# Kernel tuning notes

Hardware: AMD Instinct MI355X
Metric: run time of the kernel (lower is better)

Reference implementation:

```python
import jax, jax.numpy as jnp
import numpy as np

NEG_INF = float('-inf')

def setup_inputs() -> dict:
    key = jax.random.key(0)
    k1, k2 = jax.random.split(key)
    B, T, S, H, D = 2, 2048, 2048, 8, 64
    q = jax.random.normal(k1, (B, T, H, D), dtype=jnp.float32)
    kv = jax.random.normal(k2, (B, S, 2, H, D), dtype=jnp.float32)
    key_padding_mask = jnp.ones((B, S), dtype=bool)  # True = valid key
    return {"q": q, "kv": kv, "key_padding_mask": key_padding_mask, "causal": 1}


def reference(q, kv, key_padding_mask, causal):
    # q: (B,T,H,D), kv: (B,S,2,H,D)
    k = kv[:, :, 0]  # (B,S,H,D)
    v = kv[:, :, 1]  # (B,S,H,D)
    D = q.shape[-1]
    scale = D ** (-0.5)
    # scores: (B,H,T,S)
    scores = jnp.einsum('bthd,bshd->bhts', q, k) * scale
    # mask: True means "mask out" (matches torch masked_fill semantics)
    mask = ~key_padding_mask[:, None, None, :]  # (B,1,1,S)
    if causal:
        T, S = scores.shape[2], scores.shape[3]
        causal_mask = jnp.triu(jnp.ones((T, S), dtype=bool), k=1)  # (T,S)
        mask = mask | causal_mask[None, None, :, :]
    scores = jnp.where(mask, NEG_INF, scores)
    attn = jax.nn.softmax(scores, axis=-1)
    out = jnp.einsum('bhts,bshd->bthd', attn, v)  # (B,T,H,D)
    return out
```

## Files before the change

### kernel.cpp

```cpp
#include <hip/hip_runtime.h>
#include <hip/hip_bf16.h>

typedef __bf16 bf8_t __attribute__((ext_vector_type(8)));
typedef float  f4_t  __attribute__((ext_vector_type(4)));
typedef int    i4_t  __attribute__((ext_vector_type(4)));

constexpr int Bc = 2;
constexpr int Tc = 2048;
constexpr int Sc = 2048;
constexpr int Hc = 8;
constexpr int Dc = 64;
constexpr int BQ = 128;
constexpr int BK = 32;
constexpr int nQB = Tc / BQ;
constexpr int NKT = Sc / BK;
constexpr int NP  = nQB / 2;
constexpr int NS  = 4;
constexpr int TILE_H = 4096;
constexpr int KH = 2048;
constexpr int SLOT_H = 8192;

__device__ __forceinline__ void g2l16(const void* g, void* l) {
    __builtin_amdgcn_global_load_lds(
        (const __attribute__((address_space(1))) void*)g,
        (__attribute__((address_space(3))) void*)l, 16, 0, 0);
}

__device__ __forceinline__ int pack_bf16(float lo, float hi) {
    const unsigned l16 = (unsigned)__builtin_bit_cast(unsigned short, (__bf16)lo);
    const unsigned h16 = (unsigned)__builtin_bit_cast(unsigned short, (__bf16)hi);
    return (int)(l16 | (h16 << 16));
}

__global__ __launch_bounds__(256)
void fa_prep(const float* __restrict__ kv, const int* __restrict__ kpm,
             __bf16* __restrict__ kvb, unsigned* __restrict__ kpmw)
{
    const int idx    = blockIdx.x * 256 + threadIdx.x;
    const int tile   = idx >> 9;
    const int within = idx & 511;
    const int b  = tile >> 9;
    const int h  = (tile >> 6) & 7;
    const int s0 = (tile & 63) * BK;
    bf8_t o;
    __bf16* dst;
    if (within < 256) {
        const int row = within >> 3;
        const int col = ((within & 7) * 8) ^ ((row & 7) << 3);
        const float* src = kv + (((size_t)(b * Sc + s0 + row) * 2 + 0) * Hc + h) * Dc + col;
        const float4 x0 = *(const float4*)src;
        const float4 x1 = *(const float4*)(src + 4);
        o[0] = (__bf16)x0.x; o[1] = (__bf16)x0.y; o[2] = (__bf16)x0.z; o[3] = (__bf16)x0.w;
        o[4] = (__bf16)x1.x; o[5] = (__bf16)x1.y; o[6] = (__bf16)x1.z; o[7] = (__bf16)x1.w;
        dst = kvb + (size_t)tile * TILE_H + within * 8;
    } else {
        const int c    = within - 256;
        const int vrow = c >> 2;
        const int g8   = c & 3;
        const float* src = kv + (((size_t)(b * Sc + s0 + g8 * 8) * 2 + 1) * Hc + h) * Dc + vrow;
        #pragma unroll
        for (int j = 0; j < 8; ++j) o[j] = (__bf16)src[(size_t)j * 2 * Hc * Dc];
        const int r  = vrow >> 1;
        const int gg = ((vrow & 1) * 4 + g8) ^ (r & 7);
        dst = kvb + (size_t)tile * TILE_H + KH + r * 64 + gg * 8;
    }
    *(bf8_t*)dst = o;

    if (idx < Bc * NKT) {
        const int bb = idx >> 6, tt = idx & 63;
        unsigned m = 0;
        for (int k = 0; k < 32; ++k)
            m |= (kpm[bb * Sc + tt * BK + k] != 0 ? 1u : 0u) << k;
        kpmw[idx] = m;
    }
}

__global__ __launch_bounds__(512, 4)
void fa_part(const float* __restrict__ q,
             const __bf16* __restrict__ kvb,
             const unsigned* __restrict__ kpmw,
             const int* __restrict__ causal_p,
             float* __restrict__ part_o,
             float* __restrict__ part_l)
{
    __shared__ __bf16 shKV[2 * SLOT_H];

    const int tid  = threadIdx.x;
    const int wave = tid >> 6;
    const int lane = tid & 63;
    const int n16  = lane & 15;
    const int quad = lane >> 4;

    const int bid = blockIdx.x;
    const int h   = bid & 7;
    const int g   = bid >> 3;
    const int b   = g / (NP * NS);
    const int rem = g % (NP * NS);
    const int p   = rem / NS;
    const int s   = rem % NS;
    const int causal = causal_p[0];

    const int nA   = causal ? (32 - 2 * p) : 32;
    const int nB   = causal ? (2 * p + 2)  : 32;
    const int ntot = nA + nB;
    const int lo   = (ntot * s + NS - 1) / NS;
    const int hi   = (ntot * (s + 1) + NS - 1) / NS;

    const __bf16* kvt = kvb + (size_t)((b * Hc + h) * NKT) * TILE_H;
    const unsigned* mw_b = kpmw + b * NKT;

    const int kA_off = n16 * 64 + ((quad * 8) ^ ((n16 & 7) << 3));
    const int vRd    = (n16 >> 1) * 64 +
                       ((((n16 & 1) << 2) | quad) ^ (n16 >> 1)) * 8;
    const int img    = tid >> 8;
    const int c8     = (tid & 255) * 8;
    const int srcK   = img * TILE_H + c8;
    const int srcV   = img * TILE_H + KH + c8;
    const int ldsK   = img * 2048 + c8;
    const int ldsV   = 4096 + img * 2048 + c8;
    const int addrA  = (n16 + ((quad & 1) << 5)) << 2;
    const int addrB  = addrA + 64;
    const bool hiQ   = quad >= 2;
    const float scale = 0.125f;

    #pragma unroll 1
    for (int seg = 0; seg < 2; ++seg) {
        const int qt = seg ? p : (nQB - 1 - p);
        const int t0 = seg ? (max(lo, nA) - nA) : lo;
        const int t1 = seg ? (hi - nA)          : min(hi, nA);
        if (t0 >= t1) continue;

        __syncthreads();

        const int q_base = qt * BQ;
        const int tqn    = q_base + wave * 16 + n16;

        bf8_t a_q[2];
        {
            const float* qrow = q + ((size_t)(b * Tc + tqn) * Hc + h) * Dc;
            #pragma unroll
            for (int f = 0; f < 2; ++f) {
                const float4 x0 = *(const float4*)(qrow + f * 32 + quad * 8);
                const float4 x1 = *(const float4*)(qrow + f * 32 + quad * 8 + 4);
                bf8_t v;
                v[0] = (__bf16)(x0.x * scale); v[1] = (__bf16)(x0.y * scale);
                v[2] = (__bf16)(x0.z * scale); v[3] = (__bf16)(x0.w * scale);
                v[4] = (__bf16)(x1.x * scale); v[5] = (__bf16)(x1.y * scale);
                v[6] = (__bf16)(x1.z * scale); v[7] = (__bf16)(x1.w * scale);
                a_q[f] = v;
            }
        }

        f4_t o_acc[4];
        #pragma unroll
        for (int dt = 0; dt < 4; ++dt) o_acc[dt] = (f4_t){0.f, 0.f, 0.f, 0.f};
        float lsum = 0.f;

        int cu = 0;
        unsigned cm0, cm1;
        {
            const __bf16* src = kvt + (size_t)(2 * t0) * TILE_H;
            g2l16(src + srcK, &shKV[ldsK]);
            g2l16(src + srcV, &shKV[ldsV]);
            cm0 = mw_b[2 * t0];
            cm1 = mw_b[2 * t0 + 1];
        }

        for (int it = t0; it < t1; ++it) {
            asm volatile("s_waitcnt vmcnt(0)" ::: "memory");
            __builtin_amdgcn_s_barrier();

            const int nx = cu ^ SLOT_H;
            unsigned nm0 = 0, nm1 = 0;
            if (it + 1 < t1) {
                const __bf16* srcn = kvt + (size_t)(2 * (it + 1)) * TILE_H;
                g2l16(srcn + srcK, &shKV[nx + ldsK]);
                g2l16(srcn + srcV, &shKV[nx + ldsV]);
                nm0 = mw_b[2 * it + 2];
                nm1 = mw_b[2 * it + 3];
            }

            const int kb = it * 64;
            #pragma unroll
            for (int hh = 0; hh < 2; ++hh) {
                const unsigned cmw = hh ? cm1 : cm0;
                int pk[2][2];
                #pragma unroll
                for (int sub = 0; sub < 2; ++sub) {
                    const int kbase = cu + hh * 2048 + sub * 1024;
                    const bf8_t bk0 = *(const bf8_t*)&shKV[kbase + kA_off];
                    const bf8_t bk1 = *(const bf8_t*)&shKV[kbase + (kA_off ^ 32)];
                    f4_t acc = (f4_t){0.f, 0.f, 0.f, 0.f};
                    acc = __builtin_amdgcn_mfma_f32_16x16x32_bf16(bk0, a_q[0], acc, 0, 0, 0);
                    acc = __builtin_amdgcn_mfma_f32_16x16x32_bf16(bk1, a_q[1], acc, 0, 0, 0);
                    const int keyb = kb + hh * 32 + sub * 16 + quad * 4;
                    const unsigned mb = cmw >> (sub * 16 + quad * 4);
                    float pv[4];
                    #pragma unroll
                    for (int r = 0; r < 4; ++r) {
                        const bool valid = ((mb >> r) & 1u) && (!causal || keyb + r <= tqn);
                        const float pp = valid ? __expf(acc[r] - 8.0f) : 0.0f;
                        lsum += pp;
                        pv[r] = pp;
                    }
                    pk[sub][0] = pack_bf16(pv[0], pv[1]);
                    pk[sub][1] = pack_bf16(pv[2], pv[3]);
                }

                const int a0 = __builtin_amdgcn_ds_bpermute(addrA, pk[0][0]);
                const int a1 = __builtin_amdgcn_ds_bpermute(addrA, pk[0][1]);
                const int b0 = __builtin_amdgcn_ds_bpermute(addrB, pk[0][0]);
                const int b1 = __builtin_amdgcn_ds_bpermute(addrB, pk[0][1]);
                const int c0 = __builtin_amdgcn_ds_bpermute(addrA, pk[1][0]);
                const int c1 = __builtin_amdgcn_ds_bpermute(addrA, pk[1][1]);
                const int d0 = __builtin_amdgcn_ds_bpermute(addrB, pk[1][0]);
                const int d1 = __builtin_amdgcn_ds_bpermute(addrB, pk[1][1]);
                union { i4_t i; bf8_t b; } u;
                u.i[0] = hiQ ? c0 : a0;
                u.i[1] = hiQ ? c1 : a1;
                u.i[2] = hiQ ? d0 : b0;
                u.i[3] = hiQ ? d1 : b1;
                const bf8_t a_p = u.b;

                const int vb = cu + 4096 + hh * 2048 + vRd;
                const bf8_t bv0 = *(const bf8_t*)&shKV[vb];
                const bf8_t bv1 = *(const bf8_t*)&shKV[vb + 512];
                const bf8_t bv2 = *(const bf8_t*)&shKV[vb + 1024];
                const bf8_t bv3 = *(const bf8_t*)&shKV[vb + 1536];
                o_acc[0] = __builtin_amdgcn_mfma_f32_16x16x32_bf16(a_p, bv0, o_acc[0], 0, 0, 0);
                o_acc[1] = __builtin_amdgcn_mfma_f32_16x16x32_bf16(a_p, bv1, o_acc[1], 0, 0, 0);
                o_acc[2] = __builtin_amdgcn_mfma_f32_16x16x32_bf16(a_p, bv2, o_acc[2], 0, 0, 0);
                o_acc[3] = __builtin_amdgcn_mfma_f32_16x16x32_bf16(a_p, bv3, o_acc[3], 0, 0, 0);
            }

            cm0 = nm0; cm1 = nm1; cu = nx;
        }

        lsum += __shfl_xor(lsum, 16);
        lsum += __shfl_xor(lsum, 32);
        float l_row[4];
        #pragma unroll
        for (int r = 0; r < 4; ++r) {
            const int li = __builtin_amdgcn_ds_bpermute((quad * 4 + r) << 2,
                                                        __builtin_bit_cast(int, lsum));
            l_row[r] = __builtin_bit_cast(float, li);
        }

        const size_t slot = (size_t)(((b * Hc + h) * NP + p) * NS + s) * 2 + seg;
        float* po = part_o + slot * (BQ * Dc);
        #pragma unroll
        for (int dt = 0; dt < 4; ++dt) {
            #pragma unroll
            for (int r = 0; r < 4; ++r) {
                const int row = wave * 16 + quad * 4 + r;
                po[row * Dc + dt * 16 + n16] = o_acc[dt][r];
            }
        }
        if (n16 == 0) {
            #pragma unroll
            for (int r = 0; r < 4; ++r) {
                const int row = wave * 16 + quad * 4 + r;
                part_l[slot * BQ + row] = l_row[r];
            }
        }
    }
}

__global__ __launch_bounds__(256, 4)
void fa_reduce(const float* __restrict__ part_o,
               const float* __restrict__ part_l,
               const int* __restrict__ causal_p,
               float* __restrict__ out)
{
    const int gtid = blockIdx.x * 256 + threadIdx.x;
    const int e    = gtid & (BQ * Dc / 4 - 1);
    const int qi   = gtid >> 11;
    const int row  = e >> 4;
    const int d4   = e & 15;

    const int qt = qi & (nQB - 1);
    const int h  = (qi >> 4) & (Hc - 1);
    const int b  = qi >> 7;
    const int causal = causal_p[0];

    const int p    = (qt < NP) ? qt : (nQB - 1 - qt);
    const int seg  = (qt < NP) ? 1 : 0;
    const int nA   = causal ? (32 - 2 * p) : 32;
    const int nB   = causal ? (2 * p + 2)  : 32;
    const int ntot = nA + nB;
    const int segLo = seg ? nA : 0;
    const int segHi = seg ? ntot : nA;

    float4 acc = make_float4(0.f, 0.f, 0.f, 0.f);
    float  l   = 0.f;
    #pragma unroll
    for (int s = 0; s < NS; ++s) {
        const int lo = (ntot * s + NS - 1) / NS;
        const int hi = (ntot * (s + 1) + NS - 1) / NS;
        if (lo < segHi && segLo < hi && lo < hi) {
            const size_t slot = (size_t)(((b * Hc + h) * NP + p) * NS + s) * 2 + seg;
            const float4 v = *(const float4*)(part_o + slot * (BQ * Dc) + row * Dc + d4 * 4);
            acc.x += v.x; acc.y += v.y; acc.z += v.z; acc.w += v.w;
            l += part_l[slot * BQ + row];
        }
    }
    const float inv = 1.0f / l;
    const int t = qt * BQ + row;
    float4 o;
    o.x = acc.x * inv; o.y = acc.y * inv; o.z = acc.z * inv; o.w = acc.w * inv;
    *(float4*)(out + ((size_t)(b * Tc + t) * Hc + h) * Dc + d4 * 4) = o;
}

extern "C" void kernel_launch(void* const* d_in, const int* in_sizes, int n_in,
                              void* d_out, int out_size, void* d_ws, size_t ws_size,
                              hipStream_t stream) {
    const float* q   = (const float*)d_in[0];
    const float* kv  = (const float*)d_in[1];
    const int*   kpm = (const int*)d_in[2];
    const int*   cz  = (const int*)d_in[3];
    float*       out = (float*)d_out;

    __bf16* kvb = (__bf16*)d_ws;
    const size_t kvb_bytes = (size_t)Bc * Hc * NKT * TILE_H * sizeof(__bf16);
    unsigned* kpmw = (unsigned*)((char*)d_ws + kvb_bytes);
    float* part_o  = (float*)((char*)d_ws + kvb_bytes + 4096);

    const size_t nslots = (size_t)Bc * Hc * NP * NS * 2;
    float* part_l = part_o + nslots * (BQ * Dc);

    const int grid0 = Bc * Hc * NKT * 512 / 256;
    fa_prep<<<grid0, 256, 0, stream>>>(kv, kpm, kvb, kpmw);

    const int grid1 = Bc * Hc * NP * NS;
    fa_part<<<grid1, 512, 0, stream>>>(q, kvb, kpmw, cz, part_o, part_l);

    const int grid2 = (int)((size_t)Bc * Hc * nQB * (BQ * Dc / 4) / 256);
    fa_reduce<<<grid2, 256, 0, stream>>>(part_o, part_l, cz, out);
}
```

Before: 111.8 us.

## Switch attention inner loop to 32x32x16 MFMA with 4 waves per block

Replaces the 16x16x32 bf16 MFMA tiles with 32x32x16 tiles, so each wave handles 32 query rows and the block shrinks from 8 to 4 waves. Scores come out in a layout the PV MFMA can consume directly, which removes the ds_bpermute shuffles for P and for the row-sum broadcast. To make that work, the V-tile layout written by the prep kernel changes to a new key permutation and swizzle. Each block now handles more rows per wave, which raises register pressure and gives fewer waves to hide latency.

```diff
diff --git a/kernel.cpp b/kernel.cpp
--- a/kernel.cpp
+++ b/kernel.cpp
@@ -3,6 +3,7 @@
 
 typedef __bf16 bf8_t __attribute__((ext_vector_type(8)));
 typedef float  f4_t  __attribute__((ext_vector_type(4)));
+typedef float  f16_t __attribute__((ext_vector_type(16)));
 typedef int    i4_t  __attribute__((ext_vector_type(4)));
 
 constexpr int Bc = 2;
@@ -30,6 +31,11 @@
     const unsigned l16 = (unsigned)__builtin_bit_cast(unsigned short, (__bf16)lo);
     const unsigned h16 = (unsigned)__builtin_bit_cast(unsigned short, (__bf16)hi);
     return (int)(l16 | (h16 << 16));
+}
+
+__device__ __forceinline__ int rho(int pos) {
+    const int t = (pos >> 2) & 3;
+    return pos + (t == 1 ? 4 : (t == 2 ? -4 : 0));
 }
 
 __global__ __launch_bounds__(256)
@@ -54,15 +60,17 @@
         o[4] = (__bf16)x1.x; o[5] = (__bf16)x1.y; o[6] = (__bf16)x1.z; o[7] = (__bf16)x1.w;
         dst = kvb + (size_t)tile * TILE_H + within * 8;
     } else {
-        const int c    = within - 256;
-        const int vrow = c >> 2;
-        const int g8   = c & 3;
-        const float* src = kv + (((size_t)(b * Sc + s0 + g8 * 8) * 2 + 1) * Hc + h) * Dc + vrow;
+        const int c  = within - 256;
+        const int d  = c >> 2;
+        const int g8 = c & 3;
+        const float* vbase = kv + (((size_t)(b * Sc + s0) * 2 + 1) * Hc + h) * Dc + d;
         #pragma unroll
-        for (int j = 0; j < 8; ++j) o[j] = (__bf16)src[(size_t)j * 2 * Hc * Dc];
-        const int r  = vrow >> 1;
-        const int gg = ((vrow & 1) * 4 + g8) ^ (r & 7);
-        dst = kvb + (size_t)tile * TILE_H + KH + r * 64 + gg * 8;
+        for (int j = 0; j < 8; ++j) {
+            const int key = rho(g8 * 8 + j);
+            o[j] = (__bf16)vbase[(size_t)key * 2 * Hc * Dc];
+        }
+        const int slot = (((d & 3) << 2) | g8) ^ ((d >> 2) & 15);
+        dst = kvb + (size_t)tile * TILE_H + KH + (d >> 2) * 128 + slot * 8;
     }
     *(bf8_t*)dst = o;
 
@@ -75,7 +83,7 @@
     }
 }
 
-__global__ __launch_bounds__(512, 4)
+__global__ __launch_bounds__(256, 2)
 void fa_part(const float* __restrict__ q,
              const __bf16* __restrict__ kvb,
              const unsigned* __restrict__ kpmw,
@@ -88,8 +96,9 @@
     const int tid  = threadIdx.x;
     const int wave = tid >> 6;
     const int lane = tid & 63;
-    const int n16  = lane & 15;
-    const int quad = lane >> 4;
+    const int qcol = lane & 31;
+    const int hi   = lane >> 5;
+    const int hi4  = hi * 4;
 
     const int bid = blockIdx.x;
     const int h   = bid & 7;
@@ -104,64 +113,72 @@
     const int nB   = causal ? (2 * p + 2)  : 32;
     const int ntot = nA + nB;
     const int lo   = (ntot * s + NS - 1) / NS;
-    const int hi   = (ntot * (s + 1) + NS - 1) / NS;
+    const int hi_s = (ntot * (s + 1) + NS - 1) / NS;
 
     const __bf16* kvt = kvb + (size_t)((b * Hc + h) * NKT) * TILE_H;
     const unsigned* mw_b = kpmw + b * NKT;
 
-    const int kA_off = n16 * 64 + ((quad * 8) ^ ((n16 & 7) << 3));
-    const int vRd    = (n16 >> 1) * 64 +
-                       ((((n16 & 1) << 2) | quad) ^ (n16 >> 1)) * 8;
-    const int img    = tid >> 8;
-    const int c8     = (tid & 255) * 8;
-    const int srcK   = img * TILE_H + c8;
-    const int srcV   = img * TILE_H + KH + c8;
-    const int ldsK   = img * 2048 + c8;
-    const int ldsV   = 4096 + img * 2048 + c8;
-    const int addrA  = (n16 + ((quad & 1) << 5)) << 2;
-    const int addrB  = addrA + 64;
-    const bool hiQ   = quad >= 2;
+    int kaddr[4];
+    #pragma unroll
+    for (int dc = 0; dc < 4; ++dc)
+        kaddr[dc] = qcol * 64 + ((((2 * dc + hi) << 3)) ^ ((qcol & 7) << 3));
+    int vaddr[2][2];
+    #pragma unroll
+    for (int kc = 0; kc < 2; ++kc)
+        #pragma unroll
+        for (int dg = 0; dg < 2; ++dg) {
+            const int d    = dg * 32 + qcol;
+            const int koct = kc * 2 + hi;
+            const int r    = d >> 2;
+            const int slot = (((d & 3) << 2) | koct) ^ (r & 15);
+            vaddr[kc][dg]  = r * 128 + slot * 8;
+        }
+    const int c8 = tid * 8;
     const float scale = 0.125f;
 
     #pragma unroll 1
     for (int seg = 0; seg < 2; ++seg) {
         const int qt = seg ? p : (nQB - 1 - p);
         const int t0 = seg ? (max(lo, nA) - nA) : lo;
-        const int t1 = seg ? (hi - nA)          : min(hi, nA);
+        const int t1 = seg ? (hi_s - nA)        : min(hi_s, nA);
         if (t0 >= t1) continue;
 
         __syncthreads();
 
         const int q_base = qt * BQ;
-        const int tqn    = q_base + wave * 16 + n16;
-
-        bf8_t a_q[2];
+        const int tqn    = q_base + wave * 32 + qcol;
+
+        bf8_t a_q[4];
         {
             const float* qrow = q + ((size_t)(b * Tc + tqn) * Hc + h) * Dc;
             #pragma unroll
-            for (int f = 0; f < 2; ++f) {
-                const float4 x0 = *(const float4*)(qrow + f * 32 + quad * 8);
-                const float4 x1 = *(const float4*)(qrow + f * 32 + quad * 8 + 4);
+            for (int dc = 0; dc < 4; ++dc) {
+                const float4 x0 = *(const float4*)(qrow + dc * 16 + hi * 8);
+                const float4 x1 = *(const float4*)(qrow + dc * 16 + hi * 8 + 4);
                 bf8_t v;
                 v[0] = (__bf16)(x0.x * scale); v[1] = (__bf16)(x0.y * scale);
                 v[2] = (__bf16)(x0.z * scale); v[3] = (__bf16)(x0.w * scale);
                 v[4] = (__bf16)(x1.x * scale); v[5] = (__bf16)(x1.y * scale);
                 v[6] = (__bf16)(x1.z * scale); v[7] = (__bf16)(x1.w * scale);
-                a_q[f] = v;
+                a_q[dc] = v;
             }
         }
 
-        f4_t o_acc[4];
+        f16_t o_acc[2];
         #pragma unroll
-        for (int dt = 0; dt < 4; ++dt) o_acc[dt] = (f4_t){0.f, 0.f, 0.f, 0.f};
+        for (int dg = 0; dg < 2; ++dg)
+            #pragma unroll
+            for (int i = 0; i < 16; ++i) o_acc[dg][i] = 0.f;
         float lsum = 0.f;
 
         int cu = 0;
         unsigned cm0, cm1;
         {
             const __bf16* src = kvt + (size_t)(2 * t0) * TILE_H;
-            g2l16(src + srcK, &shKV[ldsK]);
-            g2l16(src + srcV, &shKV[ldsV]);
+            g2l16(src + c8,               &shKV[c8]);
+            g2l16(src + TILE_H + c8,      &shKV[2048 + c8]);
+            g2l16(src + KH + c8,          &shKV[4096 + c8]);
+            g2l16(src + TILE_H + KH + c8, &shKV[6144 + c8]);
             cm0 = mw_b[2 * t0];
             cm1 = mw_b[2 * t0 + 1];
         }
@@ -174,95 +191,67 @@
             unsigned nm0 = 0, nm1 = 0;
             if (it + 1 < t1) {
                 const __bf16* srcn = kvt + (size_t)(2 * (it + 1)) * TILE_H;
-                g2l16(srcn + srcK, &shKV[nx + ldsK]);
-                g2l16(srcn + srcV, &shKV[nx + ldsV]);
+                g2l16(srcn + c8,               &shKV[nx + c8]);
+                g2l16(srcn + TILE_H + c8,      &shKV[nx + 2048 + c8]);
+                g2l16(srcn + KH + c8,          &shKV[nx + 4096 + c8]);
+                g2l16(srcn + TILE_H + KH + c8, &shKV[nx + 6144 + c8]);
                 nm0 = mw_b[2 * it + 2];
                 nm1 = mw_b[2 * it + 3];
             }
 
             const int kb = it * 64;
             #pragma unroll
-            for (int hh = 0; hh < 2; ++hh) {
-                const unsigned cmw = hh ? cm1 : cm0;
-                int pk[2][2];
-                #pragma unroll
-                for (int sub = 0; sub < 2; ++sub) {
-                    const int kbase = cu + hh * 2048 + sub * 1024;
-                    const bf8_t bk0 = *(const bf8_t*)&shKV[kbase + kA_off];
-                    const bf8_t bk1 = *(const bf8_t*)&shKV[kbase + (kA_off ^ 32)];
-                    f4_t acc = (f4_t){0.f, 0.f, 0.f, 0.f};
-                    acc = __builtin_amdgcn_mfma_f32_16x16x32_bf16(bk0, a_q[0], acc, 0, 0, 0);
-                    acc = __builtin_amdgcn_mfma_f32_16x16x32_bf16(bk1, a_q[1], acc, 0, 0, 0);
-                    const int keyb = kb + hh * 32 + sub * 16 + quad * 4;
-                    const unsigned mb = cmw >> (sub * 16 + quad * 4);
-                    float pv[4];
-                    #pragma unroll
-                    for (int r = 0; r < 4; ++r) {
-                        const bool valid = ((mb >> r) & 1u) && (!causal || keyb + r <= tqn);
-                        const float pp = valid ? __expf(acc[r] - 8.0f) : 0.0f;
-                        lsum += pp;
-                        pv[r] = pp;
-                    }
-                    pk[sub][0] = pack_bf16(pv[0], pv[1]);
-                    pk[sub][1] = pack_bf16(pv[2], pv[3]);
+            for (int kh = 0; kh < 2; ++kh) {
+                const unsigned msk = (kh ? cm1 : cm0) >> hi4;
+                f16_t sc;
+                #pragma unroll
+                for (int i = 0; i < 16; ++i) sc[i] = 0.f;
+                #pragma unroll
+                for (int dc = 0; dc < 4; ++dc) {
+                    const bf8_t bk = *(const bf8_t*)&shKV[cu + kh * 2048 + kaddr[dc]];
+                    sc = __builtin_amdgcn_mfma_f32_32x32x16_bf16(bk, a_q[dc], sc, 0, 0, 0);
                 }
-
-                const int a0 = __builtin_amdgcn_ds_bpermute(addrA, pk[0][0]);
-                const int a1 = __builtin_amdgcn_ds_bpermute(addrA, pk[0][1]);
-                const int b0 = __builtin_amdgcn_ds_bpermute(addrB, pk[0][0]);
-                const int b1 = __builtin_amdgcn_ds_bpermute(addrB, pk[0][1]);
-                const int c0 = __builtin_amdgcn_ds_bpermute(addrA, pk[1][0]);
-                const int c1 = __builtin_amdgcn_ds_bpermute(addrA, pk[1][1]);
-                const int d0 = __builtin_amdgcn_ds_bpermute(addrB, pk[1][0]);
-                const int d1 = __builtin_amdgcn_ds_bpermute(addrB, pk[1][1]);
-                union { i4_t i; bf8_t b; } u;
-                u.i[0] = hiQ ? c0 : a0;
-                u.i[1] = hiQ ? c1 : a1;
-                u.i[2] = hiQ ? d0 : b0;
-                u.i[3] = hiQ ? d1 : b1;
-                const bf8_t a_p = u.b;
-
-                const int vb = cu + 4096 + hh * 2048 + vRd;
-                const bf8_t bv0 = *(const bf8_t*)&shKV[vb];
-                const bf8_t bv1 = *(const bf8_t*)&shKV[vb + 512];
-                const bf8_t bv2 = *(const bf8_t*)&shKV[vb + 1024];
-                const bf8_t bv3 = *(const bf8_t*)&shKV[vb + 1536];
-                o_acc[0] = __builtin_amdgcn_mfma_f32_16x16x32_bf16(a_p, bv0, o_acc[0], 0, 0, 0);
-                o_acc[1] = __builtin_amdgcn_mfma_f32_16x16x32_bf16(a_p, bv1, o_acc[1], 0, 0, 0);
-                o_acc[2] = __builtin_amdgcn_mfma_f32_16x16x32_bf16(a_p, bv2, o_acc[2], 0, 0, 0);
-                o_acc[3] = __builtin_amdgcn_mfma_f32_16x16x32_bf16(a_p, bv3, o_acc[3], 0, 0, 0);
+                float pv[16];
+                #pragma unroll
+                for (int r = 0; r < 16; ++r) {
+                    const int krow = (r & 3) + 8 * (r >> 2);
+                    const int key  = kb + kh * 32 + krow + hi4;
+                    const bool valid = ((msk >> krow) & 1u) && (!causal || key <= tqn);
+                    const float pp = valid ? __expf(sc[r] - 8.0f) : 0.0f;
+                    lsum += pp;
+                    pv[r] = pp;
+                }
+                union { i4_t i; bf8_t v; } ua, ub;
+                #pragma unroll
+                for (int r2 = 0; r2 < 4; ++r2) {
+                    ua.i[r2] = pack_bf16(pv[2 * r2],     pv[2 * r2 + 1]);
+                    ub.i[r2] = pack_bf16(pv[8 + 2 * r2], pv[9 + 2 * r2]);
+                }
+                #pragma unroll
+                for (int dg = 0; dg < 2; ++dg) {
+                    const int vbase = cu + 4096 + kh * 2048;
+                    const bf8_t bv0 = *(const bf8_t*)&shKV[vbase + vaddr[0][dg]];
+                    o_acc[dg] = __builtin_amdgcn_mfma_f32_32x32x16_bf16(ua.v, bv0, o_acc[dg], 0, 0, 0);
+                    const bf8_t bv1 = *(const bf8_t*)&shKV[vbase + vaddr[1][dg]];
+                    o_acc[dg] = __builtin_amdgcn_mfma_f32_32x32x16_bf16(ub.v, bv1, o_acc[dg], 0, 0, 0);
+                }
             }
-
             cm0 = nm0; cm1 = nm1; cu = nx;
         }
 
-        lsum += __shfl_xor(lsum, 16);
         lsum += __shfl_xor(lsum, 32);
-        float l_row[4];
-        #pragma unroll
-        for (int r = 0; r < 4; ++r) {
-            const int li = __builtin_amdgcn_ds_bpermute((quad * 4 + r) << 2,
-                                                        __builtin_bit_cast(int, lsum));
-            l_row[r] = __builtin_bit_cast(float, li);
-        }
 
         const size_t slot = (size_t)(((b * Hc + h) * NP + p) * NS + s) * 2 + seg;
         float* po = part_o + slot * (BQ * Dc);
         #pragma unroll
-        for (int dt = 0; dt < 4; ++dt) {
+        for (int dg = 0; dg < 2; ++dg)
             #pragma unroll
-            for (int r = 0; r < 4; ++r) {
-                const int row = wave * 16 + quad * 4 + r;
-                po[row * Dc + dt * 16 + n16] = o_acc[dt][r];
+            for (int r = 0; r < 16; ++r) {
+                const int row = wave * 32 + (r & 3) + 8 * (r >> 2) + hi4;
+                po[row * Dc + dg * 32 + qcol] = o_acc[dg][r];
             }
-        }
-        if (n16 == 0) {
-            #pragma unroll
-            for (int r = 0; r < 4; ++r) {
-                const int row = wave * 16 + quad * 4 + r;
-                part_l[slot * BQ + row] = l_row[r];
-            }
-        }
+        if (hi == 0)
+            part_l[slot * BQ + wave * 32 + qcol] = lsum;
     }
 }
 
@@ -332,7 +321,7 @@
     fa_prep<<<grid0, 256, 0, stream>>>(kv, kpm, kvb, kpmw);
 
     const int grid1 = Bc * Hc * NP * NS;
-    fa_part<<<grid1, 512, 0, stream>>>(q, kvb, kpmw, cz, part_o, part_l);
+    fa_part<<<grid1, 256, 0, stream>>>(q, kvb, kpmw, cz, part_o, part_l);
 
     const int grid2 = (int)((size_t)Bc * Hc * nQB * (BQ * Dc / 4) / 256);
     fa_reduce<<<grid2, 256, 0, stream>>>(part_o, part_l, cz, out);
```

After: 112.0 us. Within noise of the previous version (+0.1%).
